# Optimization experiments

Hardware: AMD Instinct MI355X
Metric: run time of the kernel (lower is better)

## Reference

```python
import jax, jax.numpy as jnp
import numpy as np

B, S, D, H = 4, 2048, 1024, 16
HD = D // H
DFF = 4 * D
EPS = 1e-5


def setup_inputs() -> dict:
    key = jax.random.key(0)
    ks = jax.random.split(key, 8)
    s = 0.02
    return {
        "x": jax.random.normal(ks[0], (B, S, D), dtype=jnp.float32),
        "ln1_g": jnp.ones((D,), jnp.float32),
        "ln1_b": jnp.zeros((D,), jnp.float32),
        "Wq": jax.random.normal(ks[1], (D, D), jnp.float32) * s,
        "Wk": jax.random.normal(ks[2], (D, D), jnp.float32) * s,
        "Wv": jax.random.normal(ks[3], (D, D), jnp.float32) * s,
        "Wo": jax.random.normal(ks[4], (D, D), jnp.float32) * s,
        "ln2_g": jnp.ones((D,), jnp.float32),
        "ln2_b": jnp.zeros((D,), jnp.float32),
        "W1": jax.random.normal(ks[5], (D, DFF), jnp.float32) * s,
        "b1": jnp.zeros((DFF,), jnp.float32),
        "W2": jax.random.normal(ks[6], (DFF, D), jnp.float32) * s,
        "b2": jnp.zeros((D,), jnp.float32),
    }


def _layernorm(x, g, b):
    mu = jnp.mean(x, axis=-1, keepdims=True)
    var = jnp.var(x, axis=-1, keepdims=True)
    return (x - mu) * jax.lax.rsqrt(var + EPS) * g + b


def _block(x, ln1_g, ln1_b, Wq, Wk, Wv, Wo, ln2_g, ln2_b, W1, b1, W2, b2):
    # --- attention sub-block (pre-norm) ---
    h = _layernorm(x, ln1_g, ln1_b)
    q = (h @ Wq).reshape(B, S, H, HD)
    k = (h @ Wk).reshape(B, S, H, HD)
    v = (h @ Wv).reshape(B, S, H, HD)
    scores = jnp.einsum("bqhd,bkhd->bhqk", q, k) / np.sqrt(HD).astype(np.float32)
    causal = jnp.tril(jnp.ones((S, S), dtype=bool))
    scores = jnp.where(causal, scores, -jnp.inf)
    attn = jax.nn.softmax(scores, axis=-1)  # dropout p=0 (eval)
    ctx = jnp.einsum("bhqk,bkhd->bqhd", attn, v).reshape(B, S, D)
    x = x + ctx @ Wo
    # --- FFN sub-block (pre-norm) ---
    h = _layernorm(x, ln2_g, ln2_b)
    h = jax.nn.gelu(h @ W1 + b1, approximate=False)  # torch nn.GELU() = exact erf
    return x + (h @ W2 + b2)


def reference(x, ln1_g, ln1_b, Wq, Wk, Wv, Wo, ln2_g, ln2_b, W1, b1, W2, b2):
    return _block(x, ln1_g, ln1_b, Wq, Wk, Wv, Wo, ln2_g, ln2_b, W1, b1, W2, b2)
```

## Files before the change

kernel.cpp:

```cpp
#include <hip/hip_runtime.h>
#include <hip/hip_bf16.h>
#include <math.h>

#define NB 4
#define NS 2048
#define ND 1024
#define NH 16
#define NHD 64
#define NDFF 4096
#define QKS 3072

typedef __attribute__((ext_vector_type(8))) short bf16x8;
typedef __attribute__((ext_vector_type(4))) float f32x4;
typedef __attribute__((ext_vector_type(16))) float f32x16;
typedef __attribute__((ext_vector_type(4))) short short4v;
typedef __attribute__((ext_vector_type(4))) int i32x4;

static __device__ __forceinline__ short f2b(float f) {
  union { __hip_bfloat16 b; short s; } u;
  u.b = __float2bfloat16(f);
  return u.s;
}

static __device__ __forceinline__ int cvtpk(float lo, float hi_) {
  int r;
  asm("v_cvt_pk_bf16_f32 %0, %1, %2" : "=v"(r) : "v"(lo), "v"(hi_));
  return r;
}

static __device__ __forceinline__ float pairmax(float x) {
  auto r = __builtin_amdgcn_permlane32_swap(__float_as_uint(x), __float_as_uint(x), false, false);
  return fmaxf(__uint_as_float(r[0]), __uint_as_float(r[1]));
}
static __device__ __forceinline__ float pairsum(float x) {
  auto r = __builtin_amdgcn_permlane32_swap(__float_as_uint(x), __float_as_uint(x), false, false);
  return __uint_as_float(r[0]) + __uint_as_float(r[1]);
}

__global__ __launch_bounds__(256) void ln_kernel(
    const float* __restrict__ x, const float* __restrict__ g,
    const float* __restrict__ b, short* __restrict__ out) {
  __shared__ float red[8];
  const int row = blockIdx.x;
  const int t = threadIdx.x;
  const float* xr = x + (size_t)row * ND;
  const float4 xv = *(const float4*)(xr + t * 4);
  float s = xv.x + xv.y + xv.z + xv.w;
  float ss = xv.x * xv.x + xv.y * xv.y + xv.z * xv.z + xv.w * xv.w;
#pragma unroll
  for (int m = 32; m >= 1; m >>= 1) {
    s += __shfl_xor(s, m);
    ss += __shfl_xor(ss, m);
  }
  if ((t & 63) == 0) { red[(t >> 6) * 2] = s; red[(t >> 6) * 2 + 1] = ss; }
  __syncthreads();
  s = red[0] + red[2] + red[4] + red[6];
  ss = red[1] + red[3] + red[5] + red[7];
  const float mu = s * (1.0f / ND);
  const float var = ss * (1.0f / ND) - mu * mu;
  const float rs = rsqrtf(var + 1e-5f);
  const float4 gv = *(const float4*)(g + t * 4);
  const float4 bv = *(const float4*)(b + t * 4);
  short o[4];
  o[0] = f2b((xv.x - mu) * rs * gv.x + bv.x);
  o[1] = f2b((xv.y - mu) * rs * gv.y + bv.y);
  o[2] = f2b((xv.z - mu) * rs * gv.z + bv.z);
  o[3] = f2b((xv.w - mu) * rs * gv.w + bv.w);
  *(short4v*)(out + (size_t)row * ND + t * 4) = *(short4v*)o;
}

__global__ __launch_bounds__(256) void tcast_kernel(
    const float* __restrict__ in, short* __restrict__ out, int K, int N) {
  __shared__ float tile[32][33];
  const int n0 = blockIdx.x * 32, k0 = blockIdx.y * 32;
  const int tx = threadIdx.x & 31, ty = threadIdx.x >> 5;
#pragma unroll
  for (int i = 0; i < 32; i += 8)
    tile[ty + i][tx] = in[(size_t)(k0 + ty + i) * N + n0 + tx];
  __syncthreads();
#pragma unroll
  for (int i = 0; i < 32; i += 8)
    out[(size_t)(n0 + ty + i) * K + k0 + tx] = f2b(tile[tx][ty + i]);
}

__global__ __launch_bounds__(256) void vtrans_kernel(
    const short* __restrict__ in, short* __restrict__ out) {
  __shared__ short tile[64][72];
  const int s0 = blockIdx.x * 64, bh = blockIdx.y;
  const int bb = bh >> 4, hh = bh & 15;
  const int rr = threadIdx.x >> 3, cc = (threadIdx.x & 7) * 8;
#pragma unroll
  for (int it = 0; it < 2; ++it) {
    const int r = rr + it * 32;
    *(bf16x8*)&tile[r][cc] =
        *(const bf16x8*)&in[((size_t)(bb * NS + s0 + r)) * QKS + 2048 + hh * NHD + cc];
  }
  __syncthreads();
  const size_t ob = (size_t)bh * NHD * NS;
#pragma unroll
  for (int it = 0; it < 2; ++it) {
    const int d = rr + it * 32;
    short o[8];
#pragma unroll
    for (int j = 0; j < 8; ++j) o[j] = tile[cc + j][d];
    *(bf16x8*)&out[ob + (size_t)d * NS + s0 + cc] = *(bf16x8*)o;
  }
}

__device__ __forceinline__ void gload16(const void* g, void* l) {
  __builtin_amdgcn_global_load_lds(
      (const __attribute__((address_space(1))) unsigned int*)g,
      (__attribute__((address_space(3))) unsigned int*)l, 16, 0, 0);
}

template <int BN, int EPI>
__global__ __launch_bounds__(512, 2) void gemm8_kernel(
    const short* __restrict__ A, const short* __restrict__ Bt,
    float* __restrict__ Cf, short* __restrict__ Cb,
    const float* __restrict__ bias, const float* __restrict__ res,
    int M, int N, int K) {
  constexpr int NFRAG = BN / 64;
  constexpr int NJ = NFRAG / 2;
  constexpr int BROUNDS = BN / 64;
  constexpr int TILE = (256 + BN) * 64;
  __shared__ short lds[2][TILE];

  const int l = threadIdx.x & 63, w = threadIdx.x >> 6;
  const int wm = w >> 2, wn = w & 3;
  const int nbm = M >> 8, nbn = N / BN;
  const int nwg = nbm * nbn;
  int wg = blockIdx.x;
  wg = (wg & 7) * (nwg >> 3) + (wg >> 3);
  const int bm = wg % nbm, bn = wg / nbm;

  const int lrow = w * 8 + (l >> 3);
  const int sgl = (l & 7) ^ ((l >> 3) & 7);
  const short* Ab = A + (size_t)(bm * 256 + lrow) * K + sgl * 8;
  const short* Bb = Bt + (size_t)(bn * BN + lrow) * K + sgl * 8;

  const int fr = l & 15, fg4 = l >> 4;
  f32x4 acc[8][NFRAG] = {};

#pragma unroll
  for (int j = 0; j < 4; ++j)
    gload16(Ab + (size_t)j * 64 * K, &lds[0][(j * 64 + w * 8) * 64]);
#pragma unroll
  for (int j = 0; j < BROUNDS; ++j)
    gload16(Bb + (size_t)j * 64 * K, &lds[0][(256 + j * 64 + w * 8) * 64]);

  const int NT = K >> 6;
  int buf = 0;
  for (int t = 0; t < NT; ++t) {
    asm volatile("s_waitcnt vmcnt(0)\n\ts_barrier" ::: "memory");
    if (t + 1 < NT) {
      const short* ga = Ab + (size_t)(t + 1) * 64;
      const short* gb = Bb + (size_t)(t + 1) * 64;
      short* lb = &lds[buf ^ 1][0];
#pragma unroll
      for (int j = 0; j < 4; ++j)
        gload16(ga + (size_t)j * 64 * K, lb + (j * 64 + w * 8) * 64);
#pragma unroll
      for (int j = 0; j < BROUNDS; ++j)
        gload16(gb + (size_t)j * 64 * K, lb + (256 + j * 64 + w * 8) * 64);
    }
    const short* la = &lds[buf][0];
    bf16x8 af[8];
#pragma unroll
    for (int q = 0; q < 4; ++q) {
      const int kh = q >> 1, np = q & 1;
      if (np == 0) {
#pragma unroll
        for (int mi = 0; mi < 8; ++mi) {
          const int r = wm * 128 + mi * 16 + fr;
          af[mi] = *(const bf16x8*)&la[r * 64 + ((kh * 4 + fg4) ^ (r & 7)) * 8];
        }
      }
      bf16x8 bfr[NJ];
#pragma unroll
      for (int nj = 0; nj < NJ; ++nj) {
        const int r = wn * (BN / 4) + (np * NJ + nj) * 16 + fr;
        bfr[nj] = *(const bf16x8*)&la[(256 + r) * 64 + ((kh * 4 + fg4) ^ (r & 7)) * 8];
      }
      __builtin_amdgcn_s_setprio(1);
#pragma unroll
      for (int mi = 0; mi < 8; ++mi)
#pragma unroll
        for (int nj = 0; nj < NJ; ++nj)
          acc[mi][np * NJ + nj] = __builtin_amdgcn_mfma_f32_16x16x32_bf16(
              af[mi], bfr[nj], acc[mi][np * NJ + nj], 0, 0, 0);
      __builtin_amdgcn_s_setprio(0);
      asm volatile("s_barrier" ::: "memory");
    }
    buf ^= 1;
  }

  const int fq = (l >> 4) * 4;
  const int wrb = bm * 256 + wm * 128;
  const int wcb = bn * BN + wn * (BN / 4);
#pragma unroll
  for (int mi = 0; mi < 8; ++mi) {
#pragma unroll
    for (int ni = 0; ni < NFRAG; ++ni) {
#pragma unroll
      for (int rr = 0; rr < 4; ++rr) {
        const int row = wrb + mi * 16 + fq + rr;
        const int col = wcb + ni * 16 + fr;
        float v = acc[mi][ni][rr];
        if (EPI == 0) {
          Cb[(size_t)row * N + col] = f2b(v);
        } else if (EPI == 1) {
          Cf[(size_t)row * N + col] = v + res[(size_t)row * N + col];
        } else if (EPI == 2) {
          v += bias[col];
          v = 0.5f * v * (1.0f + erff(v * 0.70710678118f));
          Cb[(size_t)row * N + col] = f2b(v);
        } else {
          Cf[(size_t)row * N + col] = v + bias[col] + res[(size_t)row * N + col];
        }
      }
    }
  }
}

__global__ __launch_bounds__(256, 2) void attn_kernel(
    const short* __restrict__ qkv, const short* __restrict__ vt, short* __restrict__ ctx) {
  __shared__ short Kls[2][64 * 64];
  __shared__ short Vls[2][64 * 64];

  const int bid = blockIdx.x;
  const int bh = (bid & 7) * 8 + ((bid >> 3) & 7);
  const int cp = bid >> 6;
  const int bb = bh >> 4, hh = bh & 15;
  const int lane = threadIdx.x & 63, wave = threadIdx.x >> 6;
  const int ql = lane & 31, hi = lane >> 5;
  const int qbA = cp * 128 + wave * 32;
  const int qbB = (15 - cp) * 128 + wave * 32;

  bf16x8 qf[2][4];
#pragma unroll
  for (int hf = 0; hf < 2; ++hf) {
    const int qb0 = hf ? qbB : qbA;
    const size_t qrow = ((size_t)bb * NS + qb0 + ql) * QKS + hh * NHD;
#pragma unroll
    for (int st = 0; st < 4; ++st)
      qf[hf][st] = *(const bf16x8*)&qkv[qrow + st * 16 + hi * 8];
  }

  f32x16 acc[2][2] = {};
  float m_run[2] = {-1e37f, -1e37f};
  float l_run[2] = {0.f, 0.f};

  const int srow = lane >> 3;
  const int sslot = (lane & 7) ^ srow;
  const short* kbasep = qkv + (size_t)bb * NS * QKS + 1024 + hh * NHD + sslot * 8;
  const short* vbasep = vt + (size_t)bh * NHD * NS + sslot * 8;

  const int nkt = (16 - cp) * 2;
#pragma unroll
  for (int r = 0; r < 2; ++r) {
    const int row = r * 32 + wave * 8 + srow;
    gload16(kbasep + (size_t)row * QKS, &Kls[0][(r * 32 + wave * 8) * 64]);
    gload16(vbasep + (size_t)row * NS, &Vls[0][(r * 32 + wave * 8) * 64]);
  }

  int buf = 0;
  for (int jt = 0; jt < nkt; ++jt) {
    asm volatile("s_waitcnt vmcnt(0)\n\ts_barrier" ::: "memory");
    if (jt + 1 < nkt) {
      const int k0n = (jt + 1) * 64;
#pragma unroll
      for (int r = 0; r < 2; ++r) {
        const int row = r * 32 + wave * 8 + srow;
        gload16(kbasep + (size_t)(k0n + row) * QKS, &Kls[buf ^ 1][(r * 32 + wave * 8) * 64]);
        gload16(vbasep + (size_t)row * NS + k0n, &Vls[buf ^ 1][(r * 32 + wave * 8) * 64]);
      }
    }
    const int k0 = jt * 64;
    const short* Kb = &Kls[buf][0];
    const short* Vb = &Vls[buf][0];
#pragma unroll
    for (int ks = 0; ks < 2; ++ks) {
      const int kbase = k0 + ks * 32;
      if (kbase > qbB) continue;
      bf16x8 kf[4], vf[2][2];
      const int krow = ks * 32 + ql;
#pragma unroll
      for (int st = 0; st < 4; ++st)
        kf[st] = *(const bf16x8*)&Kb[krow * 64 + ((st * 2 + hi) ^ (krow & 7)) * 8];
#pragma unroll
      for (int db = 0; db < 2; ++db) {
        const int vrow = db * 32 + ql;
#pragma unroll
        for (int su = 0; su < 2; ++su)
          vf[db][su] =
              *(const bf16x8*)&Vb[vrow * 64 + ((ks * 4 + su * 2 + hi) ^ (vrow & 7)) * 8];
      }
#pragma unroll
      for (int hf = 0; hf < 2; ++hf) {
        const int qb0 = hf ? qbB : qbA;
        if (kbase > qb0) continue;
        const int qg = qb0 + ql;
        f32x16 s = {};
        __builtin_amdgcn_s_setprio(1);
#pragma unroll
        for (int st = 0; st < 4; ++st)
          s = __builtin_amdgcn_mfma_f32_32x32x16_bf16(kf[st], qf[hf][st], s, 0, 0, 0);
        __builtin_amdgcn_s_setprio(0);
        const bool masked = (kbase + 31 > qb0);
        float pv[16];
        float mt = -INFINITY;
#pragma unroll
        for (int r = 0; r < 16; ++r) {
          float v = s[r] * 0.125f;
          if (masked) {
            const int key = kbase + 4 * hi + (r & 3) + 8 * (r >> 2);
            v = (key > qg) ? -INFINITY : v;
          }
          pv[r] = v;
          mt = fmaxf(mt, v);
        }
        mt = pairmax(mt);
        if (!__all(mt - m_run[hf] <= 8.0f)) {
          const float mn = fmaxf(m_run[hf], mt);
          const float sc = __expf(m_run[hf] - mn);
          m_run[hf] = mn;
          l_run[hf] *= sc;
          acc[hf][0] *= sc;
          acc[hf][1] *= sc;
        }
        float pe[16];
        float lt = 0.f;
#pragma unroll
        for (int r = 0; r < 16; ++r) {
          pe[r] = __expf(fminf(pv[r] - m_run[hf], 80.0f));
          lt += pe[r];
        }
        l_run[hf] += pairsum(lt);
        bf16x8 pf[2];
#pragma unroll
        for (int su = 0; su < 2; ++su) {
          const int a0 = cvtpk(pe[su * 8 + 0], pe[su * 8 + 1]);
          const int a1 = cvtpk(pe[su * 8 + 2], pe[su * 8 + 3]);
          const int b0 = cvtpk(pe[su * 8 + 4], pe[su * 8 + 5]);
          const int b1 = cvtpk(pe[su * 8 + 6], pe[su * 8 + 7]);
          auto r0 = __builtin_amdgcn_permlane32_swap((unsigned)a0, (unsigned)b0, false, false);
          auto r1 = __builtin_amdgcn_permlane32_swap((unsigned)a1, (unsigned)b1, false, false);
          union { i32x4 w; bf16x8 v; } u;
          u.w[0] = r0[0]; u.w[1] = r1[0]; u.w[2] = r0[1]; u.w[3] = r1[1];
          pf[su] = u.v;
        }
        __builtin_amdgcn_s_setprio(1);
#pragma unroll
        for (int su = 0; su < 2; ++su) {
          acc[hf][0] = __builtin_amdgcn_mfma_f32_32x32x16_bf16(vf[0][su], pf[su], acc[hf][0], 0, 0, 0);
          acc[hf][1] = __builtin_amdgcn_mfma_f32_32x32x16_bf16(vf[1][su], pf[su], acc[hf][1], 0, 0, 0);
        }
        __builtin_amdgcn_s_setprio(0);
      }
    }
    asm volatile("s_waitcnt lgkmcnt(0)\n\ts_barrier" ::: "memory");
    buf ^= 1;
  }

#pragma unroll
  for (int hf = 0; hf < 2; ++hf) {
    const int qb0 = hf ? qbB : qbA;
    const float inv = 1.0f / l_run[hf];
    const size_t ob = ((size_t)bb * NS + qb0 + ql) * ND + hh * NHD + hi * 8;
#pragma unroll
    for (int db = 0; db < 2; ++db) {
#pragma unroll
      for (int J = 0; J < 2; ++J) {
        const int a0 = cvtpk(acc[hf][db][J * 8 + 0] * inv, acc[hf][db][J * 8 + 1] * inv);
        const int a1 = cvtpk(acc[hf][db][J * 8 + 2] * inv, acc[hf][db][J * 8 + 3] * inv);
        const int b0 = cvtpk(acc[hf][db][J * 8 + 4] * inv, acc[hf][db][J * 8 + 5] * inv);
        const int b1 = cvtpk(acc[hf][db][J * 8 + 6] * inv, acc[hf][db][J * 8 + 7] * inv);
        auto r0 = __builtin_amdgcn_permlane32_swap((unsigned)a0, (unsigned)b0, false, false);
        auto r1 = __builtin_amdgcn_permlane32_swap((unsigned)a1, (unsigned)b1, false, false);
        union { i32x4 w; bf16x8 v; } u;
        u.w[0] = r0[0]; u.w[1] = r1[0]; u.w[2] = r0[1]; u.w[3] = r1[1];
        *(bf16x8*)&ctx[ob + db * 32 + J * 16] = u.v;
      }
    }
  }
}

extern "C" void kernel_launch(void* const* d_in, const int* in_sizes, int n_in,
                              void* d_out, int out_size, void* d_ws, size_t ws_size,
                              hipStream_t stream) {
  (void)in_sizes; (void)n_in; (void)out_size; (void)ws_size;
  const float* x     = (const float*)d_in[0];
  const float* ln1_g = (const float*)d_in[1];
  const float* ln1_b = (const float*)d_in[2];
  const float* Wq    = (const float*)d_in[3];
  const float* Wk    = (const float*)d_in[4];
  const float* Wv    = (const float*)d_in[5];
  const float* Wo    = (const float*)d_in[6];
  const float* ln2_g = (const float*)d_in[7];
  const float* ln2_b = (const float*)d_in[8];
  const float* W1    = (const float*)d_in[9];
  const float* b1    = (const float*)d_in[10];
  const float* W2    = (const float*)d_in[11];
  const float* b2    = (const float*)d_in[12];
  float* out = (float*)d_out;

  char* ws = (char*)d_ws;
  const size_t MiB = 1024 * 1024;
  short* wqkvT = (short*)(ws + 0 * MiB);
  short* woT   = (short*)(ws + 6 * MiB);
  short* w1T   = (short*)(ws + 8 * MiB);
  short* w2T   = (short*)(ws + 16 * MiB);
  short* h     = (short*)(ws + 24 * MiB);
  short* ctx   = (short*)(ws + 24 * MiB);
  short* qkv   = (short*)(ws + 40 * MiB);
  short* vt    = (short*)(ws + 88 * MiB);
  short* hff   = (short*)(ws + 40 * MiB);
  float* x1    = (float*)(ws + 104 * MiB);

  tcast_kernel<<<dim3(32, 32), 256, 0, stream>>>(Wq, wqkvT, 1024, 1024);
  tcast_kernel<<<dim3(32, 32), 256, 0, stream>>>(Wk, wqkvT + 1024 * 1024, 1024, 1024);
  tcast_kernel<<<dim3(32, 32), 256, 0, stream>>>(Wv, wqkvT + 2048 * 1024, 1024, 1024);
  tcast_kernel<<<dim3(32, 32), 256, 0, stream>>>(Wo, woT, 1024, 1024);
  tcast_kernel<<<dim3(128, 32), 256, 0, stream>>>(W1, w1T, 1024, 4096);
  tcast_kernel<<<dim3(32, 128), 256, 0, stream>>>(W2, w2T, 4096, 1024);

  ln_kernel<<<8192, 256, 0, stream>>>(x, ln1_g, ln1_b, h);

  gemm8_kernel<256, 0><<<384, 512, 0, stream>>>(h, wqkvT, nullptr, qkv, nullptr, nullptr,
                                                8192, 3072, 1024);
  vtrans_kernel<<<dim3(32, 64), 256, 0, stream>>>(qkv, vt);

  attn_kernel<<<512, 256, 0, stream>>>(qkv, vt, ctx);

  gemm8_kernel<128, 1><<<256, 512, 0, stream>>>(ctx, woT, x1, nullptr, nullptr, x,
                                                8192, 1024, 1024);

  ln_kernel<<<8192, 256, 0, stream>>>(x1, ln2_g, ln2_b, h);

  gemm8_kernel<256, 2><<<512, 512, 0, stream>>>(h, w1T, nullptr, hff, b1, nullptr,
                                                8192, 4096, 1024);
  gemm8_kernel<128, 3><<<256, 512, 0, stream>>>(hff, w2T, out, nullptr, b2, x1,
                                                8192, 1024, 4096);
}
```

Baseline: 406.8 us.

## Restructure GEMM to triple-buffered K=32 stages with partial vmcnt waits

The GEMM kernel now uses a three-deep LDS ring with K-step 32 instead of double buffering at K-step 64. It prefetches two stages ahead and waits only for the oldest stage using partial vmcnt counts. Each wave now always owns a 128x64 output tile, so the BN=128 GEMMs launch 256 threads instead of 512. Together these remove the per-quarter barriers and hide more global-load latency, at the cost of more barriers per K and fewer waves for the narrow GEMMs.

```diff
diff --git a/kernel.cpp b/kernel.cpp
--- a/kernel.cpp
+++ b/kernel.cpp
@@ -114,93 +114,97 @@
 }
 
 template <int BN, int EPI>
-__global__ __launch_bounds__(512, 2) void gemm8_kernel(
+__global__ __launch_bounds__(BN * 2, 2) void gemmk_kernel(
     const short* __restrict__ A, const short* __restrict__ Bt,
     float* __restrict__ Cf, short* __restrict__ Cb,
     const float* __restrict__ bias, const float* __restrict__ res,
     int M, int N, int K) {
-  constexpr int NFRAG = BN / 64;
-  constexpr int NJ = NFRAG / 2;
-  constexpr int BROUNDS = BN / 64;
-  constexpr int TILE = (256 + BN) * 64;
-  __shared__ short lds[2][TILE];
-
-  const int l = threadIdx.x & 63, w = threadIdx.x >> 6;
-  const int wm = w >> 2, wn = w & 3;
-  const int nbm = M >> 8, nbn = N / BN;
-  const int nwg = nbm * nbn;
+  constexpr int WN = BN / 64;
+  constexpr int T = 128 * WN;
+  constexpr int AROUNDS = 1024 / T;
+  constexpr int BROUNDS = 2;
+  constexpr int TS = (256 + BN) * 32;
+  __shared__ short lds[3][TS];
+
+  const int tid = threadIdx.x;
+  const int l = tid & 63, w = tid >> 6;
+  const int wm = w / WN, wn = w % WN;
+  const int nbm = M >> 8, nbn = N / BN, nwg = nbm * nbn;
   int wg = blockIdx.x;
   wg = (wg & 7) * (nwg >> 3) + (wg >> 3);
   const int bm = wg % nbm, bn = wg / nbm;
 
-  const int lrow = w * 8 + (l >> 3);
-  const int sgl = (l & 7) ^ ((l >> 3) & 7);
-  const short* Ab = A + (size_t)(bm * 256 + lrow) * K + sgl * 8;
-  const short* Bb = Bt + (size_t)(bn * BN + lrow) * K + sgl * 8;
+  const int srcs = (l & 3) ^ ((l >> 2) & 3) ^ ((l >> 4) & 3);
+  const short* Asrc = A + (size_t)(bm * 256 + (tid >> 2)) * K + srcs * 8;
+  const short* Bsrc = Bt + (size_t)(bn * BN + (tid >> 2)) * K + srcs * 8;
+
+  auto stage = [&](int u, int sb) {
+    short* d = &lds[sb][0] + w * 512;
+    const short* as = Asrc + u * 32;
+    const short* bs = Bsrc + u * 32;
+#pragma unroll
+    for (int j = 0; j < AROUNDS; ++j)
+      gload16(as + (size_t)j * (T / 4) * K, d + j * T * 8);
+#pragma unroll
+    for (int j = 0; j < BROUNDS; ++j)
+      gload16(bs + (size_t)j * (T / 4) * K, d + 8192 + j * T * 8);
+  };
 
   const int fr = l & 15, fg4 = l >> 4;
-  f32x4 acc[8][NFRAG] = {};
-
-#pragma unroll
-  for (int j = 0; j < 4; ++j)
-    gload16(Ab + (size_t)j * 64 * K, &lds[0][(j * 64 + w * 8) * 64]);
-#pragma unroll
-  for (int j = 0; j < BROUNDS; ++j)
-    gload16(Bb + (size_t)j * 64 * K, &lds[0][(256 + j * 64 + w * 8) * 64]);
-
-  const int NT = K >> 6;
-  int buf = 0;
+  int aoff[8], boff[4];
+#pragma unroll
+  for (int mi = 0; mi < 8; ++mi) {
+    const int r = wm * 128 + mi * 16 + fr;
+    aoff[mi] = r * 32 + (fg4 ^ (r & 3) ^ ((r >> 2) & 3)) * 8;
+  }
+#pragma unroll
+  for (int nj = 0; nj < 4; ++nj) {
+    const int r = wn * 64 + nj * 16 + fr;
+    boff[nj] = 8192 + r * 32 + (fg4 ^ (r & 3) ^ ((r >> 2) & 3)) * 8;
+  }
+
+  f32x4 acc[8][4] = {};
+  const int NT = K >> 5;
+  stage(0, 0);
+  stage(1, 1);
+  int rb = 0;
   for (int t = 0; t < NT; ++t) {
-    asm volatile("s_waitcnt vmcnt(0)\n\ts_barrier" ::: "memory");
     if (t + 1 < NT) {
-      const short* ga = Ab + (size_t)(t + 1) * 64;
-      const short* gb = Bb + (size_t)(t + 1) * 64;
-      short* lb = &lds[buf ^ 1][0];
-#pragma unroll
-      for (int j = 0; j < 4; ++j)
-        gload16(ga + (size_t)j * 64 * K, lb + (j * 64 + w * 8) * 64);
-#pragma unroll
-      for (int j = 0; j < BROUNDS; ++j)
-        gload16(gb + (size_t)j * 64 * K, lb + (256 + j * 64 + w * 8) * 64);
-    }
-    const short* la = &lds[buf][0];
-    bf16x8 af[8];
-#pragma unroll
-    for (int q = 0; q < 4; ++q) {
-      const int kh = q >> 1, np = q & 1;
-      if (np == 0) {
-#pragma unroll
-        for (int mi = 0; mi < 8; ++mi) {
-          const int r = wm * 128 + mi * 16 + fr;
-          af[mi] = *(const bf16x8*)&la[r * 64 + ((kh * 4 + fg4) ^ (r & 7)) * 8];
-        }
-      }
-      bf16x8 bfr[NJ];
-#pragma unroll
-      for (int nj = 0; nj < NJ; ++nj) {
-        const int r = wn * (BN / 4) + (np * NJ + nj) * 16 + fr;
-        bfr[nj] = *(const bf16x8*)&la[(256 + r) * 64 + ((kh * 4 + fg4) ^ (r & 7)) * 8];
-      }
-      __builtin_amdgcn_s_setprio(1);
-#pragma unroll
-      for (int mi = 0; mi < 8; ++mi)
-#pragma unroll
-        for (int nj = 0; nj < NJ; ++nj)
-          acc[mi][np * NJ + nj] = __builtin_amdgcn_mfma_f32_16x16x32_bf16(
-              af[mi], bfr[nj], acc[mi][np * NJ + nj], 0, 0, 0);
-      __builtin_amdgcn_s_setprio(0);
-      asm volatile("s_barrier" ::: "memory");
-    }
-    buf ^= 1;
+      if constexpr (BN == 256)
+        asm volatile("s_waitcnt vmcnt(4)\n\ts_barrier" ::: "memory");
+      else
+        asm volatile("s_waitcnt vmcnt(6)\n\ts_barrier" ::: "memory");
+    } else {
+      asm volatile("s_waitcnt vmcnt(0)\n\ts_barrier" ::: "memory");
+    }
+    if (t + 2 < NT) {
+      int sb = rb + 2;
+      if (sb >= 3) sb -= 3;
+      stage(t + 2, sb);
+    }
+    const short* la = &lds[rb][0];
+    bf16x8 af[8], bf[4];
+#pragma unroll
+    for (int mi = 0; mi < 8; ++mi) af[mi] = *(const bf16x8*)(la + aoff[mi]);
+#pragma unroll
+    for (int nj = 0; nj < 4; ++nj) bf[nj] = *(const bf16x8*)(la + boff[nj]);
+    __builtin_amdgcn_s_setprio(1);
+#pragma unroll
+    for (int mi = 0; mi < 8; ++mi)
+#pragma unroll
+      for (int nj = 0; nj < 4; ++nj)
+        acc[mi][nj] = __builtin_amdgcn_mfma_f32_16x16x32_bf16(af[mi], bf[nj], acc[mi][nj], 0, 0, 0);
+    __builtin_amdgcn_s_setprio(0);
+    if (++rb == 3) rb = 0;
   }
 
   const int fq = (l >> 4) * 4;
   const int wrb = bm * 256 + wm * 128;
-  const int wcb = bn * BN + wn * (BN / 4);
+  const int wcb = bn * BN + wn * 64;
 #pragma unroll
   for (int mi = 0; mi < 8; ++mi) {
 #pragma unroll
-    for (int ni = 0; ni < NFRAG; ++ni) {
+    for (int ni = 0; ni < 4; ++ni) {
 #pragma unroll
       for (int rr = 0; rr < 4; ++rr) {
         const int row = wrb + mi * 16 + fq + rr;
@@ -426,19 +430,19 @@
 
   ln_kernel<<<8192, 256, 0, stream>>>(x, ln1_g, ln1_b, h);
 
-  gemm8_kernel<256, 0><<<384, 512, 0, stream>>>(h, wqkvT, nullptr, qkv, nullptr, nullptr,
+  gemmk_kernel<256, 0><<<384, 512, 0, stream>>>(h, wqkvT, nullptr, qkv, nullptr, nullptr,
                                                 8192, 3072, 1024);
   vtrans_kernel<<<dim3(32, 64), 256, 0, stream>>>(qkv, vt);
 
   attn_kernel<<<512, 256, 0, stream>>>(qkv, vt, ctx);
 
-  gemm8_kernel<128, 1><<<256, 512, 0, stream>>>(ctx, woT, x1, nullptr, nullptr, x,
+  gemmk_kernel<128, 1><<<256, 256, 0, stream>>>(ctx, woT, x1, nullptr, nullptr, x,
                                                 8192, 1024, 1024);
 
   ln_kernel<<<8192, 256, 0, stream>>>(x1, ln2_g, ln2_b, h);
 
-  gemm8_kernel<256, 2><<<512, 512, 0, stream>>>(h, w1T, nullptr, hff, b1, nullptr,
+  gemmk_kernel<256, 2><<<512, 512, 0, stream>>>(h, w1T, nullptr, hff, b1, nullptr,
                                                 8192, 4096, 1024);
-  gemm8_kernel<128, 3><<<256, 512, 0, stream>>>(hff, w2T, out, nullptr, b2, x1,
+  gemmk_kernel<128, 3><<<256, 256, 0, stream>>>(hff, w2T, out, nullptr, b2, x1,
                                                 8192, 1024, 4096);
 }
```

Result: slower. 427.0 us (+5.0%).

## Replace 256-row double-buffered GEMM with 128x128 single-buffer tiles

Applied to the files above, without the earlier changes.

Replaces the 512-thread GEMM (256xBN tile, double-buffered LDS with async prefetch overlapping compute) with a 256-thread 128x128 tile kernel that uses a single LDS buffer. The next K-slice is loaded only after compute finishes, behind barriers. The intent is higher occupancy (launch bounds 3 per CU) and more workgroups for better CU balance. In exchange, global loads no longer overlap MFMA work inside a block, and the smaller tiles give less data reuse per byte loaded.

```diff
diff --git a/kernel.cpp b/kernel.cpp
--- a/kernel.cpp
+++ b/kernel.cpp
@@ -113,94 +113,86 @@
       (__attribute__((address_space(3))) unsigned int*)l, 16, 0, 0);
 }
 
-template <int BN, int EPI>
-__global__ __launch_bounds__(512, 2) void gemm8_kernel(
+template <int EPI>
+__global__ __launch_bounds__(256, 3) void gemm97_kernel(
     const short* __restrict__ A, const short* __restrict__ Bt,
     float* __restrict__ Cf, short* __restrict__ Cb,
     const float* __restrict__ bias, const float* __restrict__ res,
     int M, int N, int K) {
-  constexpr int NFRAG = BN / 64;
-  constexpr int NJ = NFRAG / 2;
-  constexpr int BROUNDS = BN / 64;
-  constexpr int TILE = (256 + BN) * 64;
-  __shared__ short lds[2][TILE];
-
-  const int l = threadIdx.x & 63, w = threadIdx.x >> 6;
-  const int wm = w >> 2, wn = w & 3;
-  const int nbm = M >> 8, nbn = N / BN;
-  const int nwg = nbm * nbn;
+  __shared__ short lds[2 * 128 * 64];
+  const int tid = threadIdx.x, l = tid & 63, w = tid >> 6;
+  const int wm = w >> 1, wn = w & 1;
+  const int nbm = M >> 7, nbn = N >> 7, nwg = nbm * nbn;
   int wg = blockIdx.x;
   wg = (wg & 7) * (nwg >> 3) + (wg >> 3);
-  const int bm = wg % nbm, bn = wg / nbm;
-
-  const int lrow = w * 8 + (l >> 3);
-  const int sgl = (l & 7) ^ ((l >> 3) & 7);
-  const short* Ab = A + (size_t)(bm * 256 + lrow) * K + sgl * 8;
-  const short* Bb = Bt + (size_t)(bn * BN + lrow) * K + sgl * 8;
+  const int bm = wg / nbn, bn = wg % nbn;
+
+  const int srow = tid >> 3;
+  const int sslot = (tid & 7) ^ (srow & 7);
+  const short* Asrc = A + (size_t)(bm * 128 + srow) * K + sslot * 8;
+  const short* Bsrc = Bt + (size_t)(bn * 128 + srow) * K + sslot * 8;
+  const int wdst = w * 512;
 
   const int fr = l & 15, fg4 = l >> 4;
-  f32x4 acc[8][NFRAG] = {};
-
-#pragma unroll
-  for (int j = 0; j < 4; ++j)
-    gload16(Ab + (size_t)j * 64 * K, &lds[0][(j * 64 + w * 8) * 64]);
-#pragma unroll
-  for (int j = 0; j < BROUNDS; ++j)
-    gload16(Bb + (size_t)j * 64 * K, &lds[0][(256 + j * 64 + w * 8) * 64]);
-
+  int arow[4], brow[4];
+#pragma unroll
+  for (int i = 0; i < 4; ++i) {
+    arow[i] = wm * 64 + i * 16 + fr;
+    brow[i] = wn * 64 + i * 16 + fr;
+  }
+
+  f32x4 acc[4][4] = {};
   const int NT = K >> 6;
-  int buf = 0;
+
+#pragma unroll
+  for (int j = 0; j < 4; ++j) {
+    gload16(Asrc, &lds[j * 2048 + wdst]);
+    gload16(Bsrc, &lds[8192 + j * 2048 + wdst]);
+    Asrc += (size_t)32 * K;
+    Bsrc += (size_t)32 * K;
+  }
+  Asrc -= (size_t)128 * K;
+  Bsrc -= (size_t)128 * K;
+
   for (int t = 0; t < NT; ++t) {
-    asm volatile("s_waitcnt vmcnt(0)\n\ts_barrier" ::: "memory");
+    __syncthreads();
+#pragma unroll
+    for (int kh = 0; kh < 2; ++kh) {
+      bf16x8 af[4], bf[4];
+#pragma unroll
+      for (int i = 0; i < 4; ++i) {
+        af[i] = *(const bf16x8*)&lds[arow[i] * 64 + (((kh * 4 + fg4) ^ (arow[i] & 7)) << 3)];
+        bf[i] = *(const bf16x8*)&lds[8192 + brow[i] * 64 + (((kh * 4 + fg4) ^ (brow[i] & 7)) << 3)];
+      }
+      __builtin_amdgcn_s_setprio(1);
+#pragma unroll
+      for (int mi = 0; mi < 4; ++mi)
+#pragma unroll
+        for (int ni = 0; ni < 4; ++ni)
+          acc[mi][ni] = __builtin_amdgcn_mfma_f32_16x16x32_bf16(af[mi], bf[ni], acc[mi][ni], 0, 0, 0);
+      __builtin_amdgcn_s_setprio(0);
+    }
+    __syncthreads();
     if (t + 1 < NT) {
-      const short* ga = Ab + (size_t)(t + 1) * 64;
-      const short* gb = Bb + (size_t)(t + 1) * 64;
-      short* lb = &lds[buf ^ 1][0];
-#pragma unroll
-      for (int j = 0; j < 4; ++j)
-        gload16(ga + (size_t)j * 64 * K, lb + (j * 64 + w * 8) * 64);
-#pragma unroll
-      for (int j = 0; j < BROUNDS; ++j)
-        gload16(gb + (size_t)j * 64 * K, lb + (256 + j * 64 + w * 8) * 64);
-    }
-    const short* la = &lds[buf][0];
-    bf16x8 af[8];
-#pragma unroll
-    for (int q = 0; q < 4; ++q) {
-      const int kh = q >> 1, np = q & 1;
-      if (np == 0) {
-#pragma unroll
-        for (int mi = 0; mi < 8; ++mi) {
-          const int r = wm * 128 + mi * 16 + fr;
-          af[mi] = *(const bf16x8*)&la[r * 64 + ((kh * 4 + fg4) ^ (r & 7)) * 8];
-        }
-      }
-      bf16x8 bfr[NJ];
-#pragma unroll
-      for (int nj = 0; nj < NJ; ++nj) {
-        const int r = wn * (BN / 4) + (np * NJ + nj) * 16 + fr;
-        bfr[nj] = *(const bf16x8*)&la[(256 + r) * 64 + ((kh * 4 + fg4) ^ (r & 7)) * 8];
-      }
-      __builtin_amdgcn_s_setprio(1);
-#pragma unroll
-      for (int mi = 0; mi < 8; ++mi)
-#pragma unroll
-        for (int nj = 0; nj < NJ; ++nj)
-          acc[mi][np * NJ + nj] = __builtin_amdgcn_mfma_f32_16x16x32_bf16(
-              af[mi], bfr[nj], acc[mi][np * NJ + nj], 0, 0, 0);
-      __builtin_amdgcn_s_setprio(0);
-      asm volatile("s_barrier" ::: "memory");
-    }
-    buf ^= 1;
+      const short* a = Asrc + (size_t)(t + 1) * 64;
+      const short* b = Bsrc + (size_t)(t + 1) * 64;
+#pragma unroll
+      for (int j = 0; j < 4; ++j) {
+        gload16(a, &lds[j * 2048 + wdst]);
+        gload16(b, &lds[8192 + j * 2048 + wdst]);
+        a += (size_t)32 * K;
+        b += (size_t)32 * K;
+      }
+    }
   }
 
   const int fq = (l >> 4) * 4;
-  const int wrb = bm * 256 + wm * 128;
-  const int wcb = bn * BN + wn * (BN / 4);
-#pragma unroll
-  for (int mi = 0; mi < 8; ++mi) {
-#pragma unroll
-    for (int ni = 0; ni < NFRAG; ++ni) {
+  const int wrb = bm * 128 + wm * 64;
+  const int wcb = bn * 128 + wn * 64;
+#pragma unroll
+  for (int mi = 0; mi < 4; ++mi) {
+#pragma unroll
+    for (int ni = 0; ni < 4; ++ni) {
 #pragma unroll
       for (int rr = 0; rr < 4; ++rr) {
         const int row = wrb + mi * 16 + fq + rr;
@@ -426,19 +418,19 @@
 
   ln_kernel<<<8192, 256, 0, stream>>>(x, ln1_g, ln1_b, h);
 
-  gemm8_kernel<256, 0><<<384, 512, 0, stream>>>(h, wqkvT, nullptr, qkv, nullptr, nullptr,
-                                                8192, 3072, 1024);
+  gemm97_kernel<0><<<1536, 256, 0, stream>>>(h, wqkvT, nullptr, qkv, nullptr, nullptr,
+                                             8192, 3072, 1024);
   vtrans_kernel<<<dim3(32, 64), 256, 0, stream>>>(qkv, vt);
 
   attn_kernel<<<512, 256, 0, stream>>>(qkv, vt, ctx);
 
-  gemm8_kernel<128, 1><<<256, 512, 0, stream>>>(ctx, woT, x1, nullptr, nullptr, x,
-                                                8192, 1024, 1024);
+  gemm97_kernel<1><<<512, 256, 0, stream>>>(ctx, woT, x1, nullptr, nullptr, x,
+                                            8192, 1024, 1024);
 
   ln_kernel<<<8192, 256, 0, stream>>>(x1, ln2_g, ln2_b, h);
 
-  gemm8_kernel<256, 2><<<512, 512, 0, stream>>>(h, w1T, nullptr, hff, b1, nullptr,
-                                                8192, 4096, 1024);
-  gemm8_kernel<128, 3><<<256, 512, 0, stream>>>(hff, w2T, out, nullptr, b2, x1,
-                                                8192, 1024, 4096);
-}
+  gemm97_kernel<2><<<2048, 256, 0, stream>>>(h, w1T, nullptr, hff, b1, nullptr,
+                                             8192, 4096, 1024);
+  gemm97_kernel<3><<<512, 256, 0, stream>>>(hff, w2T, out, nullptr, b2, x1,
+                                            8192, 1024, 4096);
+}
```

Measured after the change: 364.8 us. -10.3%, faster.
